# Performance work log

Hardware: AMD Instinct MI355X
Metric: run time of the kernel (lower is better)

## Reference

```python
import jax, jax.numpy as jnp
import numpy as np

DIM = 512
HID = 1024
E = 8          # num_experts
K = 2          # num_experts_per_tok
B, S = 4, 2048


def setup_inputs() -> dict:
    key = jax.random.key(0)
    ks = jax.random.split(key, 10)
    sd = DIM ** -0.5
    sh = HID ** -0.5
    return {
        "x": jax.random.normal(ks[0], (B, S, DIM), dtype=jnp.float32),
        "gate_w": jax.random.normal(ks[1], (E, DIM), dtype=jnp.float32) * sd,
        "biases": jnp.zeros((E,), dtype=jnp.float32),  # e_expert_biases
        # routed experts: swiglu  y = (silu(x@w1) * (x@w3)) @ w2
        "w1": jax.random.normal(ks[2], (E, DIM, HID), dtype=jnp.float32) * sd,
        "w3": jax.random.normal(ks[3], (E, DIM, HID), dtype=jnp.float32) * sd,
        "w2": jax.random.normal(ks[4], (E, HID, DIM), dtype=jnp.float32) * sh,
        # single shared expert
        "sw1": jax.random.normal(ks[5], (DIM, HID), dtype=jnp.float32) * sd,
        "sw3": jax.random.normal(ks[6], (DIM, HID), dtype=jnp.float32) * sd,
        "sw2": jax.random.normal(ks[7], (HID, DIM), dtype=jnp.float32) * sh,
    }


def reference(x, gate_w, biases, w1, w3, w2, sw1, sw3, sw2):
    Bb, Ss, D = x.shape
    xt = x.reshape(Bb * Ss, D)                      # [T, D]

    # shared expert (applied to full x)
    shared = (jax.nn.silu(xt @ sw1) * (xt @ sw3)) @ sw2  # [T, D]

    # router
    scores = xt @ gate_w.T                          # [T, E]
    # indices chosen from biased scores (aux-free load balancing)
    _, idx = jax.lax.top_k(scores + biases, K)      # [T, K] int
    # gate values are top-k of the UNBIASED scores (as in original code)
    topv, _ = jax.lax.top_k(scores, K)              # [T, K]
    p = jax.nn.sigmoid(topv)
    p = p / jnp.sum(p, axis=-1, keepdims=True)      # [T, K]

    # every expert on every token (dense-combine MoE reference)
    h = jax.nn.silu(jnp.einsum('td,edh->eth', xt, w1)) * jnp.einsum('td,edh->eth', xt, w3)
    y = jnp.einsum('eth,ehd->etd', h, w2)           # [E, T, D]

    onehot = jax.nn.one_hot(idx, E, dtype=xt.dtype)  # [T, K, E]
    comb = jnp.einsum('tk,tke->te', p, onehot)       # [T, E] combine weights
    out = jnp.einsum('te,etd->td', comb, y) + shared
    return out.reshape(Bb, Ss, D)
```

## Files before the change

kernel.cpp:

```cpp
#include <hip/hip_runtime.h>
#include <hip/hip_bf16.h>


#define Tn 8192
#define Dd 512
#define Hh 1024
#define NEx 9

typedef __attribute__((ext_vector_type(8))) short short8;
typedef __attribute__((ext_vector_type(4))) float f32x4;

#define AS1 __attribute__((address_space(1)))
#define AS3 __attribute__((address_space(3)))

#define OFF_XB    ((size_t)0)
#define OFF_W13T  (OFF_XB + (size_t)Tn * Dd * 2)
#define OFF_W2T   (OFF_W13T + (size_t)NEx * 2 * Hh * Dd * 2)
#define OFF_HBUF  (OFF_W2T + (size_t)NEx * Dd * Hh * 2)
#define OFF_TOK   (OFF_HBUF + (size_t)(3 * Tn) * Hh * 2)
#define OFF_SLOTP (OFF_TOK + (size_t)8 * Tn * 4)
#define OFF_PG    (OFF_SLOTP + (size_t)Tn * 2 * 4)
#define OFF_CNT   (OFF_PG + (size_t)Tn * 2 * 4)
#define OFF_OFFS  (OFF_CNT + 1024)
#define OFF_YC    OFF_XB

__device__ __forceinline__ ushort f2bf(float f) {
    unsigned int u = __float_as_uint(f);
    return (ushort)((u + 0x7fffu + ((u >> 16) & 1u)) >> 16);
}
__device__ __forceinline__ float bf2f(short s) {
    return __uint_as_float(((unsigned int)(unsigned short)s) << 16);
}

__global__ __launch_bounds__(256) void trans_kernel(
        const float* __restrict__ w1, const float* __restrict__ sw1,
        const float* __restrict__ w3, const float* __restrict__ sw3,
        const float* __restrict__ w2, const float* __restrict__ sw2,
        ushort* __restrict__ w13t, ushort* __restrict__ w2t) {
    __shared__ float tile[32][33];
    int z = blockIdx.z;
    int fam = z / 9, sl = z - fam * 9;
    int tx = threadIdx.x & 31, ty = threadIdx.x >> 5;
    if (fam < 2) {
        const float* base = (fam == 0) ? ((sl < 8) ? w1 + (size_t)sl * Dd * Hh : sw1)
                                       : ((sl < 8) ? w3 + (size_t)sl * Dd * Hh : sw3);
        ushort* dst = w13t + (size_t)sl * 2 * Hh * Dd;
        int c0 = blockIdx.x * 32, r0 = blockIdx.y * 32;
#pragma unroll
        for (int k = 0; k < 4; ++k)
            tile[ty + 8 * k][tx] = base[(size_t)(r0 + ty + 8 * k) * Hh + c0 + tx];
        __syncthreads();
#pragma unroll
        for (int k = 0; k < 4; ++k) {
            int h = c0 + ty + 8 * k;
            int n = (((h >> 4) * 2 + fam) << 4) + (h & 15);
            dst[(size_t)n * Dd + r0 + tx] = f2bf(tile[tx][ty + 8 * k]);
        }
    } else {
        const float* base = (sl < 8) ? w2 + (size_t)sl * Dd * Hh : sw2;
        ushort* dst = w2t + (size_t)sl * Dd * Hh;
        int r0 = blockIdx.x * 32, c0 = blockIdx.y * 32;
#pragma unroll
        for (int k = 0; k < 4; ++k)
            tile[ty + 8 * k][tx] = base[(size_t)(r0 + ty + 8 * k) * Dd + c0 + tx];
        __syncthreads();
#pragma unroll
        for (int k = 0; k < 4; ++k)
            dst[(size_t)(c0 + ty + 8 * k) * Hh + r0 + tx] = f2bf(tile[tx][ty + 8 * k]);
    }
}

__global__ __launch_bounds__(256) void router_kernel(const float* __restrict__ x,
                                                     const float* __restrict__ gw,
                                                     const float* __restrict__ bias,
                                                     int* __restrict__ cnt,
                                                     int* __restrict__ tok,
                                                     int* __restrict__ slotp,
                                                     float* __restrict__ pg,
                                                     ushort* __restrict__ xb) {
    __shared__ int le[64];
    __shared__ float lg[64];
    __shared__ int lpos[64];
    __shared__ int lcnt[8];
    __shared__ int gbase[8];
    int tid = threadIdx.x, lane = tid & 63, wave = tid >> 6;
    if (tid < 8) lcnt[tid] = 0;
    __syncthreads();
    int t0 = blockIdx.x * 32 + wave * 8;
    for (int it = 0; it < 8; ++it) {
        int t = t0 + it;
        const float4* xr = (const float4*)(x + (size_t)t * Dd);
        float4 xa = xr[lane * 2], xc = xr[lane * 2 + 1];
        ushort4 o1, o2;
        o1.x = f2bf(xa.x); o1.y = f2bf(xa.y); o1.z = f2bf(xa.z); o1.w = f2bf(xa.w);
        o2.x = f2bf(xc.x); o2.y = f2bf(xc.y); o2.z = f2bf(xc.z); o2.w = f2bf(xc.w);
        *(ushort4*)(xb + (size_t)t * Dd + lane * 8) = o1;
        *(ushort4*)(xb + (size_t)t * Dd + lane * 8 + 4) = o2;
        float sc[8];
#pragma unroll
        for (int e = 0; e < 8; ++e) {
            const float4* gr = (const float4*)(gw + (size_t)e * Dd);
            float4 ga = gr[lane * 2], gc = gr[lane * 2 + 1];
            float s = xa.x * ga.x + xa.y * ga.y + xa.z * ga.z + xa.w * ga.w
                    + xc.x * gc.x + xc.y * gc.y + xc.z * gc.z + xc.w * gc.w;
#pragma unroll
            for (int o = 32; o > 0; o >>= 1) s += __shfl_xor(s, o);
            sc[e] = s;
        }
        if (lane == 0) {
            float b0 = -1e30f; int i0 = 0;
#pragma unroll
            for (int e = 0; e < 8; ++e) { float bv = sc[e] + bias[e]; if (bv > b0) { b0 = bv; i0 = e; } }
            float b1v = -1e30f; int i1 = (i0 == 0) ? 1 : 0;
#pragma unroll
            for (int e = 0; e < 8; ++e) if (e != i0) { float bv = sc[e] + bias[e]; if (bv > b1v) { b1v = bv; i1 = e; } }
            float v0 = -1e30f; int k0i = 0;
#pragma unroll
            for (int e = 0; e < 8; ++e) if (sc[e] > v0) { v0 = sc[e]; k0i = e; }
            float v1 = -1e30f;
#pragma unroll
            for (int e = 0; e < 8; ++e) if (e != k0i && sc[e] > v1) v1 = sc[e];
            float p0 = 1.f / (1.f + __expf(-v0));
            float p1 = 1.f / (1.f + __expf(-v1));
            float inv = 1.f / (p0 + p1);
            int ai = (wave * 8 + it) * 2;
            le[ai] = i0;     lg[ai] = p0 * inv;
            le[ai + 1] = i1; lg[ai + 1] = p1 * inv;
        }
    }
    __syncthreads();
    if (tid < 64) lpos[tid] = atomicAdd(&lcnt[le[tid]], 1);
    __syncthreads();
    if (tid < 8) gbase[tid] = atomicAdd(&cnt[tid * 32], lcnt[tid]);
    __syncthreads();
    if (tid < 64) {
        int e = le[tid];
        int dst = gbase[e] + lpos[tid];
        int t = blockIdx.x * 32 + (tid >> 1);
        tok[(size_t)e * Tn + dst] = t;
        slotp[t * 2 + (tid & 1)] = (e << 16) | dst;
        pg[t * 2 + (tid & 1)] = lg[tid];
    }
}

__global__ void scan_kernel(const int* cnt, int* off, int* cntc) {
    if (threadIdx.x == 0 && blockIdx.x == 0) {
        int s = 0;
        for (int e = 0; e < 8; ++e) { int c = cnt[e * 32]; cntc[e] = c; off[e] = s; s += c; }
        off[8] = s;
        cntc[8] = Tn;
    }
}

__global__ __launch_bounds__(256, 2) void stage1_kernel(
        const ushort* __restrict__ xb, const ushort* __restrict__ w13t,
        const int* __restrict__ tok, const int* __restrict__ cntc,
        const int* __restrict__ off, ushort* __restrict__ Hbuf) {
    int e = blockIdx.z;
    int cn = cntc[e];
    int m0 = blockIdx.x * 128;
    if (m0 >= cn) return;
    int n0 = blockIdx.y * 128;
    const ushort* we = w13t + (size_t)e * 2 * Hh * Dd;

    __shared__ ushort As[128 * 64];
    __shared__ ushort Bs[128 * 64];
    __shared__ int toks[128];

    int tid = threadIdx.x;
    if (tid < 128) {
        int slot = m0 + tid;
        int sl = slot < cn ? slot : cn - 1;
        toks[tid] = (e == 8) ? sl : tok[(size_t)e * Tn + sl];
    }
    __syncthreads();

    int lane = tid & 63, wave = tid >> 6;
    int wm = (wave & 1) * 64, wn = (wave >> 1) * 64;
    int col15 = lane & 15, quad = lane >> 4;
    int lr = lane >> 3;
    int lcx = ((lane & 7) ^ lr) * 8;

    f32x4 acc[4][4];
#pragma unroll
    for (int a = 0; a < 4; ++a)
#pragma unroll
        for (int b = 0; b < 4; ++b) acc[a][b] = (f32x4){0.f, 0.f, 0.f, 0.f};

    for (int kb = 0; kb < Dd; kb += 64) {
#pragma unroll
        for (int i = 0; i < 4; ++i) {
            int cid = wave * 4 + i;
            const ushort* g = xb + (size_t)toks[cid * 8 + lr] * Dd + kb + lcx;
            __builtin_amdgcn_global_load_lds((const AS1 void*)g, (AS3 void*)(As + cid * 512), 16, 0, 0);
        }
#pragma unroll
        for (int i = 0; i < 4; ++i) {
            int cid = wave * 4 + i;
            const ushort* g = we + (size_t)(n0 + cid * 8 + lr) * Dd + kb + lcx;
            __builtin_amdgcn_global_load_lds((const AS1 void*)g, (AS3 void*)(Bs + cid * 512), 16, 0, 0);
        }
        __syncthreads();
#pragma unroll
        for (int ks = 0; ks < 2; ++ks) {
            int px = ((ks * 4 + quad) ^ (col15 & 7)) * 8;
            short8 a[4], b[4];
#pragma unroll
            for (int mi = 0; mi < 4; ++mi)
                a[mi] = *(const short8*)&As[(wm + mi * 16 + col15) * 64 + px];
#pragma unroll
            for (int ni = 0; ni < 4; ++ni)
                b[ni] = *(const short8*)&Bs[(wn + ni * 16 + col15) * 64 + px];
#pragma unroll
            for (int mi = 0; mi < 4; ++mi)
#pragma unroll
                for (int ni = 0; ni < 4; ++ni)
                    acc[mi][ni] = __builtin_amdgcn_mfma_f32_16x16x32_bf16(a[mi], b[ni], acc[mi][ni], 0, 0, 0);
        }
        __syncthreads();
    }

    int oe = off[e];
    int hbase = (n0 + wn) >> 1;
#pragma unroll
    for (int mi = 0; mi < 4; ++mi)
#pragma unroll
        for (int r = 0; r < 4; ++r) {
            int slot = m0 + wm + mi * 16 + quad * 4 + r;
            if (slot < cn) {
                size_t rowb = (size_t)(oe + slot) * Hh;
#pragma unroll
                for (int np = 0; np < 2; ++np) {
                    float h1 = acc[mi][np * 2][r], h3 = acc[mi][np * 2 + 1][r];
                    float s = h1 / (1.f + __expf(-h1));
                    Hbuf[rowb + hbase + np * 16 + col15] = f2bf(s * h3);
                }
            }
        }
}

__global__ __launch_bounds__(256, 3) void stage2_kernel(
        const ushort* __restrict__ Hbuf, const ushort* __restrict__ w2t,
        const int* __restrict__ cntc, const int* __restrict__ off,
        ushort* __restrict__ Yc) {
    int e = blockIdx.z;
    int cn = cntc[e];
    int m0 = blockIdx.x * 128;
    if (m0 >= cn) return;
    int n0 = blockIdx.y * 128;
    int oe = off[e];
    const ushort* w2e = w2t + (size_t)e * Dd * Hh;

    __shared__ ushort As[128 * 64];
    __shared__ ushort Bs[128 * 64];

    int tid = threadIdx.x;
    int lane = tid & 63, wave = tid >> 6;
    int wm = (wave & 1) * 64, wn = (wave >> 1) * 64;
    int col15 = lane & 15, quad = lane >> 4;
    int lr = lane >> 3;
    int lcx = ((lane & 7) ^ lr) * 8;

    f32x4 acc[4][4];
#pragma unroll
    for (int a = 0; a < 4; ++a)
#pragma unroll
        for (int b = 0; b < 4; ++b) acc[a][b] = (f32x4){0.f, 0.f, 0.f, 0.f};

    for (int kb = 0; kb < Hh; kb += 64) {
#pragma unroll
        for (int i = 0; i < 4; ++i) {
            int cid = wave * 4 + i;
            const ushort* g = Hbuf + (size_t)(oe + m0 + cid * 8 + lr) * Hh + kb + lcx;
            __builtin_amdgcn_global_load_lds((const AS1 void*)g, (AS3 void*)(As + cid * 512), 16, 0, 0);
        }
#pragma unroll
        for (int i = 0; i < 4; ++i) {
            int cid = wave * 4 + i;
            const ushort* g = w2e + (size_t)(n0 + cid * 8 + lr) * Hh + kb + lcx;
            __builtin_amdgcn_global_load_lds((const AS1 void*)g, (AS3 void*)(Bs + cid * 512), 16, 0, 0);
        }
        __syncthreads();
#pragma unroll
        for (int ks = 0; ks < 2; ++ks) {
            int px = ((ks * 4 + quad) ^ (col15 & 7)) * 8;
            short8 a[4], b[4];
#pragma unroll
            for (int mi = 0; mi < 4; ++mi)
                a[mi] = *(const short8*)&As[(wm + mi * 16 + col15) * 64 + px];
#pragma unroll
            for (int ni = 0; ni < 4; ++ni)
                b[ni] = *(const short8*)&Bs[(wn + ni * 16 + col15) * 64 + px];
#pragma unroll
            for (int mi = 0; mi < 4; ++mi)
#pragma unroll
                for (int ni = 0; ni < 4; ++ni)
                    acc[mi][ni] = __builtin_amdgcn_mfma_f32_16x16x32_bf16(a[mi], b[ni], acc[mi][ni], 0, 0, 0);
        }
        __syncthreads();
    }

#pragma unroll
    for (int mi = 0; mi < 4; ++mi)
#pragma unroll
        for (int r = 0; r < 4; ++r) {
            int slot = m0 + wm + mi * 16 + quad * 4 + r;
            if (slot < cn) {
                size_t rowb = (size_t)(oe + slot) * Dd;
#pragma unroll
                for (int ni = 0; ni < 4; ++ni)
                    Yc[rowb + n0 + wn + ni * 16 + col15] = f2bf(acc[mi][ni][r]);
            }
        }
}

__global__ __launch_bounds__(256) void combine_kernel(const ushort* __restrict__ Yc,
        const int* __restrict__ slotp, const float* __restrict__ pg,
        const int* __restrict__ off, float* __restrict__ out) {
    int g = blockIdx.x * 256 + threadIdx.x;
    int t = g >> 6;
    int c = (g & 63) * 8;
    int p0 = slotp[t * 2], p1 = slotp[t * 2 + 1];
    float g0 = pg[t * 2], g1 = pg[t * 2 + 1];
    int s0 = off[p0 >> 16] + (p0 & 0xffff);
    int s1 = off[p1 >> 16] + (p1 & 0xffff);
    int s2 = off[8] + t;
    short8 a = *(const short8*)(Yc + (size_t)s0 * Dd + c);
    short8 b = *(const short8*)(Yc + (size_t)s1 * Dd + c);
    short8 d = *(const short8*)(Yc + (size_t)s2 * Dd + c);
    float o[8];
#pragma unroll
    for (int i = 0; i < 8; ++i)
        o[i] = g0 * bf2f(a[i]) + g1 * bf2f(b[i]) + bf2f(d[i]);
    float* dst = out + (size_t)t * Dd + c;
    *(float4*)dst = (float4){o[0], o[1], o[2], o[3]};
    *(float4*)(dst + 4) = (float4){o[4], o[5], o[6], o[7]};
}

extern "C" void kernel_launch(void* const* d_in, const int* in_sizes, int n_in,
                              void* d_out, int out_size, void* d_ws, size_t ws_size,
                              hipStream_t stream) {
    (void)in_sizes; (void)n_in; (void)out_size; (void)ws_size;
    const float* x    = (const float*)d_in[0];
    const float* gw   = (const float*)d_in[1];
    const float* bias = (const float*)d_in[2];
    const float* w1   = (const float*)d_in[3];
    const float* w3   = (const float*)d_in[4];
    const float* w2   = (const float*)d_in[5];
    const float* sw1  = (const float*)d_in[6];
    const float* sw3  = (const float*)d_in[7];
    const float* sw2  = (const float*)d_in[8];
    float* out = (float*)d_out;

    char* ws = (char*)d_ws;
    ushort* xb    = (ushort*)(ws + OFF_XB);
    ushort* w13t  = (ushort*)(ws + OFF_W13T);
    ushort* w2t   = (ushort*)(ws + OFF_W2T);
    ushort* Hbuf  = (ushort*)(ws + OFF_HBUF);
    ushort* Yc    = (ushort*)(ws + OFF_YC);
    int*    tok   = (int*)(ws + OFF_TOK);
    int*    slotp = (int*)(ws + OFF_SLOTP);
    float*  pg    = (float*)(ws + OFF_PG);
    int*    cnt   = (int*)(ws + OFF_CNT);
    int*    off   = (int*)(ws + OFF_OFFS);
    int*    cntc  = off + 16;

    hipMemsetAsync(cnt, 0, 1024, stream);

    trans_kernel<<<dim3(32, 16, 27), 256, 0, stream>>>(w1, sw1, w3, sw3, w2, sw2, w13t, w2t);
    router_kernel<<<256, 256, 0, stream>>>(x, gw, bias, cnt, tok, slotp, pg, xb);
    scan_kernel<<<1, 64, 0, stream>>>(cnt, off, cntc);

    stage1_kernel<<<dim3(64, 16, NEx), 256, 0, stream>>>(xb, w13t, tok, cntc, off, Hbuf);
    stage2_kernel<<<dim3(64, Dd / 128, NEx), 256, 0, stream>>>(Hbuf, w2t, cntc, off, Yc);
    combine_kernel<<<2048, 256, 0, stream>>>(Yc, slotp, pg, off, out);
}
```

Measured before the change: 263.0 us.

## Merge transpose and router kernels, drop scan kernel by recomputing offsets

Fuses the weight transpose/convert kernel and the router kernel into one launch, using an extra z-slice of the grid for the routing blocks. It also removes the single-thread scan kernel: each downstream kernel now recomputes the per-expert prefix offsets from the counts itself. The aim is fewer launches and serialized gaps between them, and letting routing overlap with the weight transpose. The cost is redundant offset loads in every thread of stage1, stage2 and combine, and wasted idle blocks in the extra grid slice.

```diff
diff --git a/kernel.cpp b/kernel.cpp
--- a/kernel.cpp
+++ b/kernel.cpp
@@ -21,7 +21,6 @@
 #define OFF_SLOTP (OFF_TOK + (size_t)8 * Tn * 4)
 #define OFF_PG    (OFF_SLOTP + (size_t)Tn * 2 * 4)
 #define OFF_CNT   (OFF_PG + (size_t)Tn * 2 * 4)
-#define OFF_OFFS  (OFF_CNT + 1024)
 #define OFF_YC    OFF_XB
 
 __device__ __forceinline__ ushort f2bf(float f) {
@@ -32,61 +31,71 @@
     return __uint_as_float(((unsigned int)(unsigned short)s) << 16);
 }
 
-__global__ __launch_bounds__(256) void trans_kernel(
+__device__ __forceinline__ void load_offsets(const int* __restrict__ cnt,
+                                             int* cvals, int* offl) {
+    int s = 0;
+#pragma unroll
+    for (int e = 0; e < 8; ++e) { cvals[e] = cnt[e * 32]; offl[e] = s; s += cvals[e]; }
+    offl[8] = s;
+    cvals[8] = Tn;
+}
+
+__global__ __launch_bounds__(256) void prep_kernel(
         const float* __restrict__ w1, const float* __restrict__ sw1,
         const float* __restrict__ w3, const float* __restrict__ sw3,
         const float* __restrict__ w2, const float* __restrict__ sw2,
-        ushort* __restrict__ w13t, ushort* __restrict__ w2t) {
+        ushort* __restrict__ w13t, ushort* __restrict__ w2t,
+        const float* __restrict__ x, const float* __restrict__ gw,
+        const float* __restrict__ bias,
+        int* __restrict__ cnt, int* __restrict__ tok,
+        int* __restrict__ slotp, float* __restrict__ pg,
+        ushort* __restrict__ xb) {
     __shared__ float tile[32][33];
-    int z = blockIdx.z;
-    int fam = z / 9, sl = z - fam * 9;
-    int tx = threadIdx.x & 31, ty = threadIdx.x >> 5;
-    if (fam < 2) {
-        const float* base = (fam == 0) ? ((sl < 8) ? w1 + (size_t)sl * Dd * Hh : sw1)
-                                       : ((sl < 8) ? w3 + (size_t)sl * Dd * Hh : sw3);
-        ushort* dst = w13t + (size_t)sl * 2 * Hh * Dd;
-        int c0 = blockIdx.x * 32, r0 = blockIdx.y * 32;
-#pragma unroll
-        for (int k = 0; k < 4; ++k)
-            tile[ty + 8 * k][tx] = base[(size_t)(r0 + ty + 8 * k) * Hh + c0 + tx];
-        __syncthreads();
-#pragma unroll
-        for (int k = 0; k < 4; ++k) {
-            int h = c0 + ty + 8 * k;
-            int n = (((h >> 4) * 2 + fam) << 4) + (h & 15);
-            dst[(size_t)n * Dd + r0 + tx] = f2bf(tile[tx][ty + 8 * k]);
-        }
-    } else {
-        const float* base = (sl < 8) ? w2 + (size_t)sl * Dd * Hh : sw2;
-        ushort* dst = w2t + (size_t)sl * Dd * Hh;
-        int r0 = blockIdx.x * 32, c0 = blockIdx.y * 32;
-#pragma unroll
-        for (int k = 0; k < 4; ++k)
-            tile[ty + 8 * k][tx] = base[(size_t)(r0 + ty + 8 * k) * Dd + c0 + tx];
-        __syncthreads();
-#pragma unroll
-        for (int k = 0; k < 4; ++k)
-            dst[(size_t)(c0 + ty + 8 * k) * Hh + r0 + tx] = f2bf(tile[tx][ty + 8 * k]);
-    }
-}
-
-__global__ __launch_bounds__(256) void router_kernel(const float* __restrict__ x,
-                                                     const float* __restrict__ gw,
-                                                     const float* __restrict__ bias,
-                                                     int* __restrict__ cnt,
-                                                     int* __restrict__ tok,
-                                                     int* __restrict__ slotp,
-                                                     float* __restrict__ pg,
-                                                     ushort* __restrict__ xb) {
     __shared__ int le[64];
     __shared__ float lg[64];
     __shared__ int lpos[64];
     __shared__ int lcnt[8];
     __shared__ int gbase[8];
-    int tid = threadIdx.x, lane = tid & 63, wave = tid >> 6;
+    int z = blockIdx.z;
+    int tid = threadIdx.x;
+    if (z < 27) {
+        int fam = z / 9, sl = z - fam * 9;
+        int tx = tid & 31, ty = tid >> 5;
+        if (fam < 2) {
+            const float* base = (fam == 0) ? ((sl < 8) ? w1 + (size_t)sl * Dd * Hh : sw1)
+                                           : ((sl < 8) ? w3 + (size_t)sl * Dd * Hh : sw3);
+            ushort* dst = w13t + (size_t)sl * 2 * Hh * Dd;
+            int c0 = blockIdx.x * 32, r0 = blockIdx.y * 32;
+#pragma unroll
+            for (int k = 0; k < 4; ++k)
+                tile[ty + 8 * k][tx] = base[(size_t)(r0 + ty + 8 * k) * Hh + c0 + tx];
+            __syncthreads();
+#pragma unroll
+            for (int k = 0; k < 4; ++k) {
+                int h = c0 + ty + 8 * k;
+                int n = (((h >> 4) * 2 + fam) << 4) + (h & 15);
+                dst[(size_t)n * Dd + r0 + tx] = f2bf(tile[tx][ty + 8 * k]);
+            }
+        } else {
+            const float* base = (sl < 8) ? w2 + (size_t)sl * Dd * Hh : sw2;
+            ushort* dst = w2t + (size_t)sl * Dd * Hh;
+            int r0 = blockIdx.x * 32, c0 = blockIdx.y * 32;
+#pragma unroll
+            for (int k = 0; k < 4; ++k)
+                tile[ty + 8 * k][tx] = base[(size_t)(r0 + ty + 8 * k) * Dd + c0 + tx];
+            __syncthreads();
+#pragma unroll
+            for (int k = 0; k < 4; ++k)
+                dst[(size_t)(c0 + ty + 8 * k) * Hh + r0 + tx] = f2bf(tile[tx][ty + 8 * k]);
+        }
+        return;
+    }
+    if (blockIdx.y >= 8) return;
+    int bid = blockIdx.y * 32 + blockIdx.x;
+    int lane = tid & 63, wave = tid >> 6;
     if (tid < 8) lcnt[tid] = 0;
     __syncthreads();
-    int t0 = blockIdx.x * 32 + wave * 8;
+    int t0 = bid * 32 + wave * 8;
     for (int it = 0; it < 8; ++it) {
         int t = t0 + it;
         const float4* xr = (const float4*)(x + (size_t)t * Dd);
@@ -136,28 +145,21 @@
     if (tid < 64) {
         int e = le[tid];
         int dst = gbase[e] + lpos[tid];
-        int t = blockIdx.x * 32 + (tid >> 1);
+        int t = bid * 32 + (tid >> 1);
         tok[(size_t)e * Tn + dst] = t;
         slotp[t * 2 + (tid & 1)] = (e << 16) | dst;
         pg[t * 2 + (tid & 1)] = lg[tid];
     }
 }
 
-__global__ void scan_kernel(const int* cnt, int* off, int* cntc) {
-    if (threadIdx.x == 0 && blockIdx.x == 0) {
-        int s = 0;
-        for (int e = 0; e < 8; ++e) { int c = cnt[e * 32]; cntc[e] = c; off[e] = s; s += c; }
-        off[8] = s;
-        cntc[8] = Tn;
-    }
-}
-
 __global__ __launch_bounds__(256, 2) void stage1_kernel(
         const ushort* __restrict__ xb, const ushort* __restrict__ w13t,
-        const int* __restrict__ tok, const int* __restrict__ cntc,
-        const int* __restrict__ off, ushort* __restrict__ Hbuf) {
+        const int* __restrict__ tok, const int* __restrict__ cnt,
+        ushort* __restrict__ Hbuf) {
     int e = blockIdx.z;
-    int cn = cntc[e];
+    int cvals[9], offl[9];
+    load_offsets(cnt, cvals, offl);
+    int cn = cvals[e];
     int m0 = blockIdx.x * 128;
     if (m0 >= cn) return;
     int n0 = blockIdx.y * 128;
@@ -220,7 +222,7 @@
         __syncthreads();
     }
 
-    int oe = off[e];
+    int oe = offl[e];
     int hbase = (n0 + wn) >> 1;
 #pragma unroll
     for (int mi = 0; mi < 4; ++mi)
@@ -241,14 +243,15 @@
 
 __global__ __launch_bounds__(256, 3) void stage2_kernel(
         const ushort* __restrict__ Hbuf, const ushort* __restrict__ w2t,
-        const int* __restrict__ cntc, const int* __restrict__ off,
-        ushort* __restrict__ Yc) {
+        const int* __restrict__ cnt, ushort* __restrict__ Yc) {
     int e = blockIdx.z;
-    int cn = cntc[e];
+    int cvals[9], offl[9];
+    load_offsets(cnt, cvals, offl);
+    int cn = cvals[e];
     int m0 = blockIdx.x * 128;
     if (m0 >= cn) return;
     int n0 = blockIdx.y * 128;
-    int oe = off[e];
+    int oe = offl[e];
     const ushort* w2e = w2t + (size_t)e * Dd * Hh;
 
     __shared__ ushort As[128 * 64];
@@ -316,15 +319,17 @@
 
 __global__ __launch_bounds__(256) void combine_kernel(const ushort* __restrict__ Yc,
         const int* __restrict__ slotp, const float* __restrict__ pg,
-        const int* __restrict__ off, float* __restrict__ out) {
+        const int* __restrict__ cnt, float* __restrict__ out) {
+    int cvals[9], offl[9];
+    load_offsets(cnt, cvals, offl);
     int g = blockIdx.x * 256 + threadIdx.x;
     int t = g >> 6;
     int c = (g & 63) * 8;
     int p0 = slotp[t * 2], p1 = slotp[t * 2 + 1];
     float g0 = pg[t * 2], g1 = pg[t * 2 + 1];
-    int s0 = off[p0 >> 16] + (p0 & 0xffff);
-    int s1 = off[p1 >> 16] + (p1 & 0xffff);
-    int s2 = off[8] + t;
+    int s0 = offl[p0 >> 16] + (p0 & 0xffff);
+    int s1 = offl[p1 >> 16] + (p1 & 0xffff);
+    int s2 = offl[8] + t;
     short8 a = *(const short8*)(Yc + (size_t)s0 * Dd + c);
     short8 b = *(const short8*)(Yc + (size_t)s1 * Dd + c);
     short8 d = *(const short8*)(Yc + (size_t)s2 * Dd + c);
@@ -362,16 +367,14 @@
     int*    slotp = (int*)(ws + OFF_SLOTP);
     float*  pg    = (float*)(ws + OFF_PG);
     int*    cnt   = (int*)(ws + OFF_CNT);
-    int*    off   = (int*)(ws + OFF_OFFS);
-    int*    cntc  = off + 16;
 
     hipMemsetAsync(cnt, 0, 1024, stream);
 
-    trans_kernel<<<dim3(32, 16, 27), 256, 0, stream>>>(w1, sw1, w3, sw3, w2, sw2, w13t, w2t);
-    router_kernel<<<256, 256, 0, stream>>>(x, gw, bias, cnt, tok, slotp, pg, xb);
-    scan_kernel<<<1, 64, 0, stream>>>(cnt, off, cntc);
-
-    stage1_kernel<<<dim3(64, 16, NEx), 256, 0, stream>>>(xb, w13t, tok, cntc, off, Hbuf);
-    stage2_kernel<<<dim3(64, Dd / 128, NEx), 256, 0, stream>>>(Hbuf, w2t, cntc, off, Yc);
-    combine_kernel<<<2048, 256, 0, stream>>>(Yc, slotp, pg, off, out);
-}
+    prep_kernel<<<dim3(32, 16, 28), 256, 0, stream>>>(w1, sw1, w3, sw3, w2, sw2,
+                                                      w13t, w2t, x, gw, bias,
+                                                      cnt, tok, slotp, pg, xb);
+
+    stage1_kernel<<<dim3(64, 16, NEx), 256, 0, stream>>>(xb, w13t, tok, cnt, Hbuf);
+    stage2_kernel<<<dim3(64, Dd / 128, NEx), 256, 0, stream>>>(Hbuf, w2t, cnt, Yc);
+    combine_kernel<<<2048, 256, 0, stream>>>(Yc, slotp, pg, cnt, out);
+}
```

New measurement: 271.9 us. 1.03x slower.
